# Performance work log

Measured on AMD Instinct MI355X. Metric: run time of the kernel, lower is better.

The kernel has to match this reference:

```python
import jax, jax.numpy as jnp
import numpy as np

DIM, NH, NKV, HD = 4096, 32, 8, 128
N_REP = NH // NKV
START_POS = 32767  # decode position; cache holds positions [0, START_POS)


def _rope(x, cos, sin):
    # x: (B, L, H, D); cos/sin: (L, D/2). Complex multiply on (even, odd) pairs.
    b, l, h, d = x.shape
    xr = x.reshape(b, l, h, d // 2, 2)
    x0, x1 = xr[..., 0], xr[..., 1]
    c = cos[None, :, None, :]
    s = sin[None, :, None, :]
    o0 = x0 * c - x1 * s
    o1 = x0 * s + x1 * c
    return jnp.stack([o0, o1], axis=-1).reshape(b, l, h, d)


def setup_inputs() -> dict:
    key = jax.random.key(0)
    ks = jax.random.split(key, 8)
    x = jax.random.normal(ks[0], (1, 1, DIM), jnp.float32)
    # real RoPE angles for the current position
    inv_freq = 1.0 / (10000.0 ** (np.arange(0, HD, 2, dtype=np.float32) / HD))
    ang = jnp.asarray((START_POS * inv_freq)[None, :], jnp.float32)  # (1, 64)
    freqs_cos = jnp.cos(ang)
    freqs_sin = jnp.sin(ang)
    k_cache = jax.random.normal(ks[1], (START_POS, NKV, HD), jnp.float32)
    v_cache = jax.random.normal(ks[2], (START_POS, NKV, HD), jnp.float32)
    sd = 1.0 / np.sqrt(DIM)
    wq = jax.random.normal(ks[3], (NH * HD, DIM), jnp.float32) * sd
    wk = jax.random.normal(ks[4], (NKV * HD, DIM), jnp.float32) * sd
    wv = jax.random.normal(ks[5], (NKV * HD, DIM), jnp.float32) * sd
    wo = jax.random.normal(ks[6], (DIM, NH * HD), jnp.float32) * sd
    return {"x": x, "freqs_cos": freqs_cos, "freqs_sin": freqs_sin,
            "k_cache": k_cache, "v_cache": v_cache,
            "wq": wq, "wk": wk, "wv": wv, "wo": wo,
            "start_pos": START_POS}


def reference(x, freqs_cos, freqs_sin, k_cache, v_cache, wq, wk, wv, wo, start_pos):
    bsz, seqlen, _ = x.shape  # (1, 1, DIM)
    q = (x @ wq.T).reshape(bsz, seqlen, NH, HD)
    k = (x @ wk.T).reshape(bsz, seqlen, NKV, HD)
    v = (x @ wv.T).reshape(bsz, seqlen, NKV, HD)
    q = _rope(q, freqs_cos, freqs_sin)
    k = _rope(k, freqs_cos, freqs_sin)
    # push current token KV and fetch full history (offloader fetch over all
    # blocks 0..start_pos//BLOCK == plain concat of cache + current token)
    k_full = jnp.concatenate([k_cache, k[0]], axis=0)  # (T, NKV, HD), T = start_pos+1
    v_full = jnp.concatenate([v_cache, v[0]], axis=0)
    # GQA repeat_kv: (T, NKV, HD) -> (1, NH, T, HD)
    T = k_full.shape[0]
    k_h = jnp.repeat(k_full, N_REP, axis=1).transpose(1, 0, 2)[None]  # (1, NH, T, HD)
    v_h = jnp.repeat(v_full, N_REP, axis=1).transpose(1, 0, 2)[None]
    qh = q.transpose(0, 2, 1, 3)  # (1, NH, 1, HD)
    scores = jnp.einsum("bhqd,bhtd->bhqt", qh, k_h) / jnp.sqrt(jnp.float32(HD))
    probs = jax.nn.softmax(scores, axis=-1)
    out = jnp.einsum("bhqt,bhtd->bhqd", probs, v_h)  # (1, NH, 1, HD)
    out = out.transpose(0, 2, 1, 3).reshape(bsz, seqlen, NH * HD)
    return out @ wo.T
```

## Files before the change

kernel.cpp:

```cpp
#include <hip/hip_runtime.h>
#include <math.h>

#define DIM 4096
#define NH 32
#define NKV 8
#define HD 128
#define NREP 4
#define PBLK 1024
#define PWAVE 256
#define TILE 8
#define NTW (PWAVE / TILE)
#define NBUF 4
#define BUF_F 2048
#define WAVE_F (NBUF * BUF_F)

__global__ __launch_bounds__(256) void qkv_rope_kernel(
    const float* __restrict__ x, const float* __restrict__ fc,
    const float* __restrict__ fs, const float* __restrict__ wq,
    const float* __restrict__ wk, const float* __restrict__ wv,
    float* __restrict__ q_rope, float* __restrict__ k_new,
    float* __restrict__ v_new) {
  int wave = blockIdx.x * 4 + (threadIdx.x >> 6);
  int lane = threadIdx.x & 63;
  const float* W;
  float* dst;
  int r0;
  bool rope;
  if (wave < 2048) {
    W = wq; dst = q_rope; r0 = wave * 2; rope = true;
  } else if (wave < 2560) {
    W = wk; dst = k_new; r0 = (wave - 2048) * 2; rope = true;
  } else {
    W = wv; dst = v_new; r0 = (wave - 2560) * 2; rope = false;
  }
  const float4* x4 = (const float4*)x;
  const float4* w0 = (const float4*)(W + (size_t)r0 * DIM);
  const float4* w1 = (const float4*)(W + (size_t)(r0 + 1) * DIM);
  float a0 = 0.f, a1 = 0.f;
#pragma unroll 4
  for (int c = lane; c < DIM / 4; c += 64) {
    float4 xv = x4[c];
    float4 u = w0[c];
    float4 v = w1[c];
    a0 += xv.x * u.x + xv.y * u.y + xv.z * u.z + xv.w * u.w;
    a1 += xv.x * v.x + xv.y * v.y + xv.z * v.z + xv.w * v.w;
  }
  for (int off = 32; off > 0; off >>= 1) {
    a0 += __shfl_down(a0, off, 64);
    a1 += __shfl_down(a1, off, 64);
  }
  if (lane == 0) {
    if (rope) {
      int jj = (r0 & (HD - 1)) >> 1;
      float c = fc[jj], s = fs[jj];
      dst[r0]     = a0 * c - a1 * s;
      dst[r0 + 1] = a0 * s + a1 * c;
    } else {
      dst[r0]     = a0;
      dst[r0 + 1] = a1;
    }
  }
}

#define LD4(p) (*(const float4*)(p))

#define GLL(src, dst)                                                       \
  __builtin_amdgcn_global_load_lds(                                         \
      (const __attribute__((address_space(1))) void*)(src),                 \
      (__attribute__((address_space(3))) void*)(dst), 16, 0, 0)

__device__ __forceinline__ void stage_tile(
    int n_, int w, int rhalf, int jg, int t0w, int gid, int start_pos,
    const float* k_cache, const float* v_cache, const float* k_new,
    const float* v_new, float* smem) {
  int bb = n_ & (NBUF - 1);
  float* kd = &smem[w * WAVE_F + bb * BUF_F];
  float* vd = kd + 1024;
#pragma unroll
  for (int ki = 0; ki < 4; ++ki) {
    int r = ki * 2 + rhalf;
    int tg = t0w + n_ * TILE + r;
    int soff = (jg ^ r) << 2;
    const float* sk;
    const float* sv;
    if (tg < start_pos) {
      sk = k_cache + ((size_t)tg * NKV + gid) * HD + soff;
      sv = v_cache + ((size_t)tg * NKV + gid) * HD + soff;
    } else {
      sk = k_new + gid * HD + soff;
      sv = v_new + gid * HD + soff;
    }
    GLL(sk, kd + ki * 256);
    GLL(sv, vd + ki * 256);
  }
}

__global__ __launch_bounds__(256, 1) void attn_partial_kernel(
    const float* __restrict__ q_rope, const float* __restrict__ k_cache,
    const float* __restrict__ v_cache, const float* __restrict__ k_new,
    const float* __restrict__ v_new, float* __restrict__ partial_l,
    float* __restrict__ partial_o, int start_pos, int nsplit) {
  int gid = blockIdx.x & 7;
  int split = blockIdx.x >> 3;
  int tid = threadIdx.x;
  int w = tid >> 6;
  int l = tid & 63;
  int t0w = split * PBLK + w * PWAVE;

  __shared__ float smem[4 * WAVE_F];
  __shared__ float p_lds[4][TILE][NREP];
  __shared__ float out_comb[4][NREP][HD];
  __shared__ float l_comb[4][NREP];

  int t = l & 7;
  int q8 = l >> 3;
  int j = l >> 4;
  int ds = l & 15;
  int rhalf = l >> 5;
  int jg = l & 31;

  const float scale = 0.08838834764831845f;

  float4 qf[NREP][4];
#pragma unroll
  for (int h = 0; h < NREP; ++h)
#pragma unroll
    for (int cc = 0; cc < 4; ++cc)
      qf[h][cc] = LD4(q_rope + (gid * NREP + h) * HD + q8 * 16 + cc * 4);

  float lsum[NREP] = {0.f, 0.f, 0.f, 0.f};
  float out[8] = {0.f, 0.f, 0.f, 0.f, 0.f, 0.f, 0.f, 0.f};

  asm volatile("s_waitcnt vmcnt(0)" ::: "memory");
  __builtin_amdgcn_sched_barrier(0);
  stage_tile(0, w, rhalf, jg, t0w, gid, start_pos, k_cache, v_cache, k_new,
             v_new, smem);
  stage_tile(1, w, rhalf, jg, t0w, gid, start_pos, k_cache, v_cache, k_new,
             v_new, smem);

  for (int n = 0; n < NTW; ++n) {
    stage_tile(n + 2, w, rhalf, jg, t0w, gid, start_pos, k_cache, v_cache,
               k_new, v_new, smem);
    asm volatile("s_waitcnt vmcnt(16)" ::: "memory");
    __builtin_amdgcn_sched_barrier(0);

    const float* kb = &smem[w * WAVE_F + (n & (NBUF - 1)) * BUF_F];
    float s0 = 0.f, s1 = 0.f, s2 = 0.f, s3 = 0.f;
#pragma unroll
    for (int cc = 0; cc < 4; ++cc) {
      float4 K4 = LD4(kb + t * 128 + (((q8 * 4 + cc) ^ t) << 2));
      s0 += K4.x * qf[0][cc].x + K4.y * qf[0][cc].y + K4.z * qf[0][cc].z +
            K4.w * qf[0][cc].w;
      s1 += K4.x * qf[1][cc].x + K4.y * qf[1][cc].y + K4.z * qf[1][cc].z +
            K4.w * qf[1][cc].w;
      s2 += K4.x * qf[2][cc].x + K4.y * qf[2][cc].y + K4.z * qf[2][cc].z +
            K4.w * qf[2][cc].w;
      s3 += K4.x * qf[3][cc].x + K4.y * qf[3][cc].y + K4.z * qf[3][cc].z +
            K4.w * qf[3][cc].w;
    }
#pragma unroll
    for (int m = 8; m <= 32; m <<= 1) {
      s0 += __shfl_xor(s0, m, 64);
      s1 += __shfl_xor(s1, m, 64);
      s2 += __shfl_xor(s2, m, 64);
      s3 += __shfl_xor(s3, m, 64);
    }
    int tg = t0w + n * TILE + t;
    bool valid = tg < start_pos;
    float p0 = valid ? __expf(s0 * scale) : 0.f;
    float p1 = valid ? __expf(s1 * scale) : 0.f;
    float p2 = valid ? __expf(s2 * scale) : 0.f;
    float p3 = valid ? __expf(s3 * scale) : 0.f;
    lsum[0] += p0; lsum[1] += p1; lsum[2] += p2; lsum[3] += p3;
    if (q8 == 0) {
      float4 pw;
      pw.x = p0; pw.y = p1; pw.z = p2; pw.w = p3;
      *(float4*)&p_lds[w][t][0] = pw;
    }
    asm volatile("s_waitcnt lgkmcnt(0)" ::: "memory");
    __builtin_amdgcn_sched_barrier(0);

    const float* vb = kb + 1024;
#pragma unroll
    for (int tt = 0; tt < TILE; ++tt) {
      float p = p_lds[w][tt][j];
      float4 Va = LD4(vb + tt * 128 + (((ds * 2) ^ tt) << 2));
      float4 Vb = LD4(vb + tt * 128 + (((ds * 2 + 1) ^ tt) << 2));
      out[0] += p * Va.x; out[1] += p * Va.y;
      out[2] += p * Va.z; out[3] += p * Va.w;
      out[4] += p * Vb.x; out[5] += p * Vb.y;
      out[6] += p * Vb.z; out[7] += p * Vb.w;
    }
  }

#pragma unroll
  for (int m = 1; m <= 4; m <<= 1) {
    lsum[0] += __shfl_xor(lsum[0], m, 64);
    lsum[1] += __shfl_xor(lsum[1], m, 64);
    lsum[2] += __shfl_xor(lsum[2], m, 64);
    lsum[3] += __shfl_xor(lsum[3], m, 64);
  }

  float4 oa, ob;
  oa.x = out[0]; oa.y = out[1]; oa.z = out[2]; oa.w = out[3];
  ob.x = out[4]; ob.y = out[5]; ob.z = out[6]; ob.w = out[7];
  *(float4*)&out_comb[w][j][ds * 8 + 0] = oa;
  *(float4*)&out_comb[w][j][ds * 8 + 4] = ob;
  if (l == 0) {
#pragma unroll
    for (int h = 0; h < NREP; ++h) l_comb[w][h] = lsum[h];
  }
  __syncthreads();
  for (int idx = tid; idx < NREP * HD; idx += 256) {
    int jj = idx >> 7, d = idx & (HD - 1);
    float s = out_comb[0][jj][d] + out_comb[1][jj][d] + out_comb[2][jj][d] +
              out_comb[3][jj][d];
    partial_o[((size_t)(gid * NREP + jj) * nsplit + split) * HD + d] = s;
  }
  if (tid < NREP) {
    partial_l[(gid * NREP + tid) * nsplit + split] =
        l_comb[0][tid] + l_comb[1][tid] + l_comb[2][tid] + l_comb[3][tid];
  }
}

__global__ __launch_bounds__(128) void combine_kernel(
    const float* __restrict__ q_rope, const float* __restrict__ k_new,
    const float* __restrict__ v_new, const float* __restrict__ partial_l,
    const float* __restrict__ partial_o, float* __restrict__ attn_out,
    int nsplit) {
  int h = blockIdx.x;
  int g = h >> 2;
  int tid = threadIdx.x;
  __shared__ float sl[512];
  __shared__ float sp[128];
  sp[tid] = q_rope[h * HD + tid] * k_new[g * HD + tid];
  for (int i = tid; i < nsplit; i += 128) sl[i] = partial_l[h * nsplit + i];
  __syncthreads();
  for (int s = 64; s > 0; s >>= 1) {
    if (tid < s) sp[tid] += sp[tid + s];
    __syncthreads();
  }
  float e_new = __expf(sp[0] * 0.08838834764831845f);
  float L = e_new;
  for (int s = 0; s < nsplit; ++s) L += sl[s];
  float acc = e_new * v_new[g * HD + tid];
#pragma unroll 4
  for (int s = 0; s < nsplit; ++s)
    acc += partial_o[((size_t)h * nsplit + s) * HD + tid];
  attn_out[h * HD + tid] = acc / L;
}

__global__ __launch_bounds__(256) void out_gemv_kernel(
    const float* __restrict__ attn, const float* __restrict__ wo,
    float* __restrict__ out) {
  int row = blockIdx.x * 4 + (threadIdx.x >> 6);
  int lane = threadIdx.x & 63;
  const float4* a4 = (const float4*)attn;
  const float4* w4 = (const float4*)(wo + (size_t)row * DIM);
  float a = 0.f;
#pragma unroll 4
  for (int c = lane; c < DIM / 4; c += 64) {
    float4 av = a4[c];
    float4 wv = w4[c];
    a += av.x * wv.x + av.y * wv.y + av.z * wv.z + av.w * wv.w;
  }
  for (int off = 32; off > 0; off >>= 1) a += __shfl_down(a, off, 64);
  if (lane == 0) out[row] = a;
}

extern "C" void kernel_launch(void* const* d_in, const int* in_sizes, int n_in,
                              void* d_out, int out_size, void* d_ws,
                              size_t ws_size, hipStream_t stream) {
  const float* x       = (const float*)d_in[0];
  const float* fc      = (const float*)d_in[1];
  const float* fs      = (const float*)d_in[2];
  const float* k_cache = (const float*)d_in[3];
  const float* v_cache = (const float*)d_in[4];
  const float* wq      = (const float*)d_in[5];
  const float* wk      = (const float*)d_in[6];
  const float* wv      = (const float*)d_in[7];
  const float* wo      = (const float*)d_in[8];
  float* out = (float*)d_out;

  int start_pos = in_sizes[3] / (NKV * HD);
  int nsplit = (start_pos + PBLK - 1) / PBLK;

  float* ws = (float*)d_ws;
  float* q_rope    = ws;
  float* k_new     = ws + 4096;
  float* v_new     = ws + 5120;
  float* attn_out  = ws + 6144;
  float* partial_l = ws + 10240;
  float* partial_o = partial_l + NH * nsplit;

  qkv_rope_kernel<<<768, 256, 0, stream>>>(x, fc, fs, wq, wk, wv, q_rope,
                                           k_new, v_new);
  attn_partial_kernel<<<NKV * nsplit, 256, 0, stream>>>(
      q_rope, k_cache, v_cache, k_new, v_new, partial_l, partial_o,
      start_pos, nsplit);
  combine_kernel<<<NH, 128, 0, stream>>>(q_rope, k_new, v_new, partial_l,
                                         partial_o, attn_out, nsplit);
  out_gemv_kernel<<<1024, 256, 0, stream>>>(attn_out, wo, out);
}
```

Measured before the change: 97.11 us.

## Split fused attention into separate score and PV kernels via global probability buffer

Replaces the single LDS-pipelined attention kernel, which staged K and V together through async global-to-LDS copies, with two kernels. A score kernel computes one token per thread, writes exp scores to a global buffer and emits per-block sums. A PV kernel then reads those probabilities and streams V directly from global memory. The aim is more parallelism and simpler, higher-occupancy memory access, at the cost of an extra launch, a probability round trip through global memory, and uncoalesced per-thread 512-byte K row reads in the score kernel.

Measured after the change: 130.3 us. 1.34x slower.

```diff
diff --git a/kernel.cpp b/kernel.cpp
--- a/kernel.cpp
+++ b/kernel.cpp
@@ -6,13 +6,10 @@
 #define NKV 8
 #define HD 128
 #define NREP 4
-#define PBLK 1024
-#define PWAVE 256
-#define TILE 8
-#define NTW (PWAVE / TILE)
-#define NBUF 4
-#define BUF_F 2048
-#define WAVE_F (NBUF * BUF_F)
+#define ABLK 512
+#define BBLK 256
+
+#define LD4(p) (*(const float4*)(p))
 
 __global__ __launch_bounds__(256) void qkv_rope_kernel(
     const float* __restrict__ x, const float* __restrict__ fc,
@@ -62,164 +59,102 @@
   }
 }
 
-#define LD4(p) (*(const float4*)(p))
-
-#define GLL(src, dst)                                                       \
-  __builtin_amdgcn_global_load_lds(                                         \
-      (const __attribute__((address_space(1))) void*)(src),                 \
-      (__attribute__((address_space(3))) void*)(dst), 16, 0, 0)
-
-__device__ __forceinline__ void stage_tile(
-    int n_, int w, int rhalf, int jg, int t0w, int gid, int start_pos,
-    const float* k_cache, const float* v_cache, const float* k_new,
-    const float* v_new, float* smem) {
-  int bb = n_ & (NBUF - 1);
-  float* kd = &smem[w * WAVE_F + bb * BUF_F];
-  float* vd = kd + 1024;
+__global__ __launch_bounds__(512, 4) void score_kernel(
+    const float* __restrict__ q_rope, const float* __restrict__ k_cache,
+    float* __restrict__ p_buf, float* __restrict__ partial_l,
+    int start_pos, int nsplit_a, int Tpad) {
+  int g = blockIdx.x & 7;
+  int blk = blockIdx.x >> 3;
+  int tid = threadIdx.x;
+  int t = blk * ABLK + tid;
+  bool valid = t < start_pos;
+  int tc = valid ? t : 0;
+  const float* kr = k_cache + ((size_t)tc * NKV + g) * HD;
+  const float* qb = q_rope + (size_t)(g * NREP) * HD;
+  float s0 = 0.f, s1 = 0.f, s2 = 0.f, s3 = 0.f;
+#pragma unroll 4
+  for (int c = 0; c < 8; ++c) {
 #pragma unroll
-  for (int ki = 0; ki < 4; ++ki) {
-    int r = ki * 2 + rhalf;
-    int tg = t0w + n_ * TILE + r;
-    int soff = (jg ^ r) << 2;
-    const float* sk;
-    const float* sv;
-    if (tg < start_pos) {
-      sk = k_cache + ((size_t)tg * NKV + gid) * HD + soff;
-      sv = v_cache + ((size_t)tg * NKV + gid) * HD + soff;
-    } else {
-      sk = k_new + gid * HD + soff;
-      sv = v_new + gid * HD + soff;
+    for (int u = 0; u < 4; ++u) {
+      int o = c * 16 + u * 4;
+      float4 K4 = LD4(kr + o);
+      float4 q0 = LD4(qb + 0 * HD + o);
+      float4 q1 = LD4(qb + 1 * HD + o);
+      float4 q2 = LD4(qb + 2 * HD + o);
+      float4 q3 = LD4(qb + 3 * HD + o);
+      s0 += K4.x * q0.x + K4.y * q0.y + K4.z * q0.z + K4.w * q0.w;
+      s1 += K4.x * q1.x + K4.y * q1.y + K4.z * q1.z + K4.w * q1.w;
+      s2 += K4.x * q2.x + K4.y * q2.y + K4.z * q2.z + K4.w * q2.w;
+      s3 += K4.x * q3.x + K4.y * q3.y + K4.z * q3.z + K4.w * q3.w;
     }
-    GLL(sk, kd + ki * 256);
-    GLL(sv, vd + ki * 256);
-  }
-}
-
-__global__ __launch_bounds__(256, 1) void attn_partial_kernel(
-    const float* __restrict__ q_rope, const float* __restrict__ k_cache,
-    const float* __restrict__ v_cache, const float* __restrict__ k_new,
-    const float* __restrict__ v_new, float* __restrict__ partial_l,
-    float* __restrict__ partial_o, int start_pos, int nsplit) {
-  int gid = blockIdx.x & 7;
+  }
+  const float scale = 0.08838834764831845f;
+  float p0 = valid ? __expf(s0 * scale) : 0.f;
+  float p1 = valid ? __expf(s1 * scale) : 0.f;
+  float p2 = valid ? __expf(s2 * scale) : 0.f;
+  float p3 = valid ? __expf(s3 * scale) : 0.f;
+  float4 pv4;
+  pv4.x = p0; pv4.y = p1; pv4.z = p2; pv4.w = p3;
+  *(float4*)&p_buf[((size_t)g * Tpad + t) * 4] = pv4;
+
+  float l0 = p0, l1 = p1, l2 = p2, l3 = p3;
+#pragma unroll
+  for (int m = 1; m <= 32; m <<= 1) {
+    l0 += __shfl_xor(l0, m, 64);
+    l1 += __shfl_xor(l1, m, 64);
+    l2 += __shfl_xor(l2, m, 64);
+    l3 += __shfl_xor(l3, m, 64);
+  }
+  __shared__ float sl[8][4];
+  int w = tid >> 6, l = tid & 63;
+  if (l == 0) {
+    sl[w][0] = l0; sl[w][1] = l1; sl[w][2] = l2; sl[w][3] = l3;
+  }
+  __syncthreads();
+  if (tid < NREP) {
+    float L = 0.f;
+#pragma unroll
+    for (int ww = 0; ww < 8; ++ww) L += sl[ww][tid];
+    partial_l[(g * NREP + tid) * nsplit_a + blk] = L;
+  }
+}
+
+__global__ __launch_bounds__(256, 4) void pv_kernel(
+    const float* __restrict__ p_buf, const float* __restrict__ v_cache,
+    float* __restrict__ partial_o, int start_pos, int nsplit_b, int Tpad) {
+  int g = blockIdx.x & 7;
   int split = blockIdx.x >> 3;
   int tid = threadIdx.x;
-  int w = tid >> 6;
-  int l = tid & 63;
-  int t0w = split * PBLK + w * PWAVE;
-
-  __shared__ float smem[4 * WAVE_F];
-  __shared__ float p_lds[4][TILE][NREP];
-  __shared__ float out_comb[4][NREP][HD];
-  __shared__ float l_comb[4][NREP];
-
-  int t = l & 7;
-  int q8 = l >> 3;
-  int j = l >> 4;
-  int ds = l & 15;
-  int rhalf = l >> 5;
-  int jg = l & 31;
-
-  const float scale = 0.08838834764831845f;
-
-  float4 qf[NREP][4];
-#pragma unroll
-  for (int h = 0; h < NREP; ++h)
-#pragma unroll
-    for (int cc = 0; cc < 4; ++cc)
-      qf[h][cc] = LD4(q_rope + (gid * NREP + h) * HD + q8 * 16 + cc * 4);
-
-  float lsum[NREP] = {0.f, 0.f, 0.f, 0.f};
+  int w = tid >> 6, l = tid & 63;
+  int h = l >> 4, ds = l & 15;
+  int tb = split * BBLK + w * 64;
+  const float* pb = p_buf + ((size_t)g * Tpad + tb) * 4 + h;
   float out[8] = {0.f, 0.f, 0.f, 0.f, 0.f, 0.f, 0.f, 0.f};
-
-  asm volatile("s_waitcnt vmcnt(0)" ::: "memory");
-  __builtin_amdgcn_sched_barrier(0);
-  stage_tile(0, w, rhalf, jg, t0w, gid, start_pos, k_cache, v_cache, k_new,
-             v_new, smem);
-  stage_tile(1, w, rhalf, jg, t0w, gid, start_pos, k_cache, v_cache, k_new,
-             v_new, smem);
-
-  for (int n = 0; n < NTW; ++n) {
-    stage_tile(n + 2, w, rhalf, jg, t0w, gid, start_pos, k_cache, v_cache,
-               k_new, v_new, smem);
-    asm volatile("s_waitcnt vmcnt(16)" ::: "memory");
-    __builtin_amdgcn_sched_barrier(0);
-
-    const float* kb = &smem[w * WAVE_F + (n & (NBUF - 1)) * BUF_F];
-    float s0 = 0.f, s1 = 0.f, s2 = 0.f, s3 = 0.f;
-#pragma unroll
-    for (int cc = 0; cc < 4; ++cc) {
-      float4 K4 = LD4(kb + t * 128 + (((q8 * 4 + cc) ^ t) << 2));
-      s0 += K4.x * qf[0][cc].x + K4.y * qf[0][cc].y + K4.z * qf[0][cc].z +
-            K4.w * qf[0][cc].w;
-      s1 += K4.x * qf[1][cc].x + K4.y * qf[1][cc].y + K4.z * qf[1][cc].z +
-            K4.w * qf[1][cc].w;
-      s2 += K4.x * qf[2][cc].x + K4.y * qf[2][cc].y + K4.z * qf[2][cc].z +
-            K4.w * qf[2][cc].w;
-      s3 += K4.x * qf[3][cc].x + K4.y * qf[3][cc].y + K4.z * qf[3][cc].z +
-            K4.w * qf[3][cc].w;
-    }
-#pragma unroll
-    for (int m = 8; m <= 32; m <<= 1) {
-      s0 += __shfl_xor(s0, m, 64);
-      s1 += __shfl_xor(s1, m, 64);
-      s2 += __shfl_xor(s2, m, 64);
-      s3 += __shfl_xor(s3, m, 64);
-    }
-    int tg = t0w + n * TILE + t;
-    bool valid = tg < start_pos;
-    float p0 = valid ? __expf(s0 * scale) : 0.f;
-    float p1 = valid ? __expf(s1 * scale) : 0.f;
-    float p2 = valid ? __expf(s2 * scale) : 0.f;
-    float p3 = valid ? __expf(s3 * scale) : 0.f;
-    lsum[0] += p0; lsum[1] += p1; lsum[2] += p2; lsum[3] += p3;
-    if (q8 == 0) {
-      float4 pw;
-      pw.x = p0; pw.y = p1; pw.z = p2; pw.w = p3;
-      *(float4*)&p_lds[w][t][0] = pw;
-    }
-    asm volatile("s_waitcnt lgkmcnt(0)" ::: "memory");
-    __builtin_amdgcn_sched_barrier(0);
-
-    const float* vb = kb + 1024;
-#pragma unroll
-    for (int tt = 0; tt < TILE; ++tt) {
-      float p = p_lds[w][tt][j];
-      float4 Va = LD4(vb + tt * 128 + (((ds * 2) ^ tt) << 2));
-      float4 Vb = LD4(vb + tt * 128 + (((ds * 2 + 1) ^ tt) << 2));
-      out[0] += p * Va.x; out[1] += p * Va.y;
-      out[2] += p * Va.z; out[3] += p * Va.w;
-      out[4] += p * Vb.x; out[5] += p * Vb.y;
-      out[6] += p * Vb.z; out[7] += p * Vb.w;
-    }
-  }
-
-#pragma unroll
-  for (int m = 1; m <= 4; m <<= 1) {
-    lsum[0] += __shfl_xor(lsum[0], m, 64);
-    lsum[1] += __shfl_xor(lsum[1], m, 64);
-    lsum[2] += __shfl_xor(lsum[2], m, 64);
-    lsum[3] += __shfl_xor(lsum[3], m, 64);
-  }
-
+#pragma unroll 4
+  for (int i = 0; i < 64; ++i) {
+    int t = tb + i;
+    int tcl = t < start_pos ? t : start_pos - 1;
+    float p = pb[i * 4];
+    const float* vr = v_cache + ((size_t)tcl * NKV + g) * HD + ds * 8;
+    float4 Va = LD4(vr);
+    float4 Vb = LD4(vr + 4);
+    out[0] += p * Va.x; out[1] += p * Va.y;
+    out[2] += p * Va.z; out[3] += p * Va.w;
+    out[4] += p * Vb.x; out[5] += p * Vb.y;
+    out[6] += p * Vb.z; out[7] += p * Vb.w;
+  }
+  __shared__ float sacc[4][NREP][HD];
   float4 oa, ob;
   oa.x = out[0]; oa.y = out[1]; oa.z = out[2]; oa.w = out[3];
   ob.x = out[4]; ob.y = out[5]; ob.z = out[6]; ob.w = out[7];
-  *(float4*)&out_comb[w][j][ds * 8 + 0] = oa;
-  *(float4*)&out_comb[w][j][ds * 8 + 4] = ob;
-  if (l == 0) {
-#pragma unroll
-    for (int h = 0; h < NREP; ++h) l_comb[w][h] = lsum[h];
-  }
+  *(float4*)&sacc[w][h][ds * 8] = oa;
+  *(float4*)&sacc[w][h][ds * 8 + 4] = ob;
   __syncthreads();
   for (int idx = tid; idx < NREP * HD; idx += 256) {
-    int jj = idx >> 7, d = idx & (HD - 1);
-    float s = out_comb[0][jj][d] + out_comb[1][jj][d] + out_comb[2][jj][d] +
-              out_comb[3][jj][d];
-    partial_o[((size_t)(gid * NREP + jj) * nsplit + split) * HD + d] = s;
-  }
-  if (tid < NREP) {
-    partial_l[(gid * NREP + tid) * nsplit + split] =
-        l_comb[0][tid] + l_comb[1][tid] + l_comb[2][tid] + l_comb[3][tid];
+    int hh = idx >> 7, d = idx & (HD - 1);
+    float s = sacc[0][hh][d] + sacc[1][hh][d] + sacc[2][hh][d] +
+              sacc[3][hh][d];
+    partial_o[((size_t)(g * NREP + hh) * nsplit_b + split) * HD + d] = s;
   }
 }
 
@@ -227,14 +162,12 @@
     const float* __restrict__ q_rope, const float* __restrict__ k_new,
     const float* __restrict__ v_new, const float* __restrict__ partial_l,
     const float* __restrict__ partial_o, float* __restrict__ attn_out,
-    int nsplit) {
-  int h = blockIdx.x;
-  int g = h >> 2;
+    int nsplit_a, int nsplit_b) {
+  int hh = blockIdx.x;
+  int g = hh >> 2;
   int tid = threadIdx.x;
-  __shared__ float sl[512];
   __shared__ float sp[128];
-  sp[tid] = q_rope[h * HD + tid] * k_new[g * HD + tid];
-  for (int i = tid; i < nsplit; i += 128) sl[i] = partial_l[h * nsplit + i];
+  sp[tid] = q_rope[hh * HD + tid] * k_new[g * HD + tid];
   __syncthreads();
   for (int s = 64; s > 0; s >>= 1) {
     if (tid < s) sp[tid] += sp[tid + s];
@@ -242,12 +175,12 @@
   }
   float e_new = __expf(sp[0] * 0.08838834764831845f);
   float L = e_new;
-  for (int s = 0; s < nsplit; ++s) L += sl[s];
+  for (int s = 0; s < nsplit_a; ++s) L += partial_l[hh * nsplit_a + s];
   float acc = e_new * v_new[g * HD + tid];
 #pragma unroll 4
-  for (int s = 0; s < nsplit; ++s)
-    acc += partial_o[((size_t)h * nsplit + s) * HD + tid];
-  attn_out[h * HD + tid] = acc / L;
+  for (int s = 0; s < nsplit_b; ++s)
+    acc += partial_o[((size_t)hh * nsplit_b + s) * HD + tid];
+  attn_out[hh * HD + tid] = acc / L;
 }
 
 __global__ __launch_bounds__(256) void out_gemv_kernel(
@@ -283,7 +216,9 @@
   float* out = (float*)d_out;
 
   int start_pos = in_sizes[3] / (NKV * HD);
-  int nsplit = (start_pos + PBLK - 1) / PBLK;
+  int nsplit_a = (start_pos + ABLK - 1) / ABLK;
+  int Tpad = nsplit_a * ABLK;
+  int nsplit_b = Tpad / BBLK;
 
   float* ws = (float*)d_ws;
   float* q_rope    = ws;
@@ -291,14 +226,17 @@
   float* v_new     = ws + 5120;
   float* attn_out  = ws + 6144;
   float* partial_l = ws + 10240;
-  float* partial_o = partial_l + NH * nsplit;
+  float* partial_o = partial_l + NH * nsplit_a;
+  float* p_buf     = partial_o + (size_t)NH * nsplit_b * HD;
 
   qkv_rope_kernel<<<768, 256, 0, stream>>>(x, fc, fs, wq, wk, wv, q_rope,
                                            k_new, v_new);
-  attn_partial_kernel<<<NKV * nsplit, 256, 0, stream>>>(
-      q_rope, k_cache, v_cache, k_new, v_new, partial_l, partial_o,
-      start_pos, nsplit);
+  score_kernel<<<8 * nsplit_a, ABLK, 0, stream>>>(
+      q_rope, k_cache, p_buf, partial_l, start_pos, nsplit_a, Tpad);
+  pv_kernel<<<8 * nsplit_b, BBLK, 0, stream>>>(
+      p_buf, v_cache, partial_o, start_pos, nsplit_b, Tpad);
   combine_kernel<<<NH, 128, 0, stream>>>(q_rope, k_new, v_new, partial_l,
-                                         partial_o, attn_out, nsplit);
+                                         partial_o, attn_out, nsplit_a,
+                                         nsplit_b);
   out_gemv_kernel<<<1024, 256, 0, stream>>>(attn_out, wo, out);
 }
```
